# Kernel optimization log

Measured on AMD Instinct MI355X. Metric: run time of the kernel, lower is better.

Reference implementation:

```python
import jax, jax.numpy as jnp
import numpy as np

N = 50000      # nodes
E = 320000     # edges (before self-loops)
DIN = 128      # embedding_dim
D = 256        # intermediate_dim
H = 4          # heads_transformer
L = 2          # transformer_layers
NEG = 0.2      # LeakyReLU slope in GATConv


def setup_inputs() -> dict:
    key = jax.random.key(0)
    ks = jax.random.split(key, 16)
    def rn(k, shape, scale=0.05):
        return jax.random.normal(k, shape, jnp.float32) * scale
    return dict(
        x=jax.random.normal(ks[0], (N, DIN), jnp.float32),
        edge_index=jax.random.randint(ks[1], (2, E), 0, N),
        gat1_W=rn(ks[2], (D, DIN)), gat1_b=jnp.zeros((D,), jnp.float32),
        gat1_asrc=rn(ks[3], (D,)), gat1_adst=rn(ks[4], (D,)),
        gat2_W=rn(ks[5], (D, D)), gat2_b=jnp.zeros((D,), jnp.float32),
        gat2_asrc=rn(ks[6], (D,)), gat2_adst=rn(ks[7], (D,)),
        cls_token=rn(ks[8], (1, D)),
        pos_emb=rn(ks[9], (3, D)),
        Wqkv=rn(ks[10], (L, 3 * D, D)), bqkv=jnp.zeros((L, 3 * D), jnp.float32),
        Wo=rn(ks[11], (L, D, D)), bo=jnp.zeros((L, D), jnp.float32),
        ln1_g=jnp.ones((L, D), jnp.float32), ln1_b=jnp.zeros((L, D), jnp.float32),
        ln2_g=jnp.ones((L, D), jnp.float32), ln2_b=jnp.zeros((L, D), jnp.float32),
        Wff1=rn(ks[12], (L, 4 * D, D)), bff1=jnp.zeros((L, 4 * D), jnp.float32),
        Wff2=rn(ks[13], (L, D, 4 * D)), bff2=jnp.zeros((L, D), jnp.float32),
        norm_g=jnp.ones((D,), jnp.float32), norm_b=jnp.zeros((D,), jnp.float32),
    )


def layer_norm(x, g, b, eps=1e-5):
    m = jnp.mean(x, -1, keepdims=True)
    v = jnp.var(x, -1, keepdims=True)
    return (x - m) * jax.lax.rsqrt(v + eps) * g + b


def gat_conv(x, src, dst, W, b, a_src, a_dst):
    # PyG GATConv, heads=1, concat=False: h = xW^T; per-edge score
    # e = LeakyReLU(<h_src, a_src> + <h_dst, a_dst>); softmax grouped by dst.
    h = x @ W.T                                            # [N, D]
    e = jax.nn.leaky_relu((h @ a_src)[src] + (h @ a_dst)[dst], NEG)  # [E']
    m = jax.ops.segment_max(e, dst, num_segments=N)
    ex = jnp.exp(e - m[dst])
    denom = jax.ops.segment_sum(ex, dst, num_segments=N)
    alpha = ex / denom[dst]
    out = jax.ops.segment_sum(alpha[:, None] * h[src], dst, num_segments=N)
    return out + b


def mha(x, Wqkv, bqkv, Wo, bo):
    B, S, _ = x.shape
    dh = D // H
    qkv = x @ Wqkv.T + bqkv                                # [B, S, 3D]
    q, k, v = jnp.split(qkv, 3, axis=-1)
    q = q.reshape(B, S, H, dh); k = k.reshape(B, S, H, dh); v = v.reshape(B, S, H, dh)
    logits = jnp.einsum('bqhd,bkhd->bhqk', q, k) / jnp.sqrt(jnp.float32(dh))
    a = jax.nn.softmax(logits, -1)
    o = jnp.einsum('bhqk,bkhd->bqhd', a, v).reshape(B, S, D)
    return o @ Wo.T + bo


def reference(x, edge_index, gat1_W, gat1_b, gat1_asrc, gat1_adst,
              gat2_W, gat2_b, gat2_asrc, gat2_adst, cls_token, pos_emb,
              Wqkv, bqkv, Wo, bo, ln1_g, ln1_b, ln2_g, ln2_b,
              Wff1, bff1, Wff2, bff2, norm_g, norm_b):
    loops = jnp.arange(N)                                   # GATConv add_self_loops=True
    src = jnp.concatenate([edge_index[0], loops])
    dst = jnp.concatenate([edge_index[1], loops])

    x1 = jax.nn.relu(gat_conv(x, src, dst, gat1_W, gat1_b, gat1_asrc, gat1_adst))
    x2 = jax.nn.relu(gat_conv(x1, src, dst, gat2_W, gat2_b, gat2_asrc, gat2_adst))

    seq = jnp.concatenate([jnp.broadcast_to(cls_token, (N, 1, D)),
                           x1[:, None, :], x2[:, None, :]], axis=1)  # [N, 3, D]
    seq = seq + pos_emb                                     # broadcast [3, D]

    # post-norm TransformerEncoder (ReLU FFN, eval mode -> no dropout)
    for l in range(L):
        seq = layer_norm(seq + mha(seq, Wqkv[l], bqkv[l], Wo[l], bo[l]), ln1_g[l], ln1_b[l])
        ff = jax.nn.relu(seq @ Wff1[l].T + bff1[l]) @ Wff2[l].T + bff2[l]
        seq = layer_norm(seq + ff, ln2_g[l], ln2_b[l])

    seq = layer_norm(seq, norm_g, norm_b)
    return seq[:, 0, :]
```

## Files before the change

kernel.cpp:

```cpp
#include <hip/hip_runtime.h>
#include <hip/hip_bf16.h>

#define NN  50000
#define EE  320000
#define E2  (EE + NN)
#define DIN 128
#define DD  256

typedef __attribute__((ext_vector_type(8))) short          bf16x8;
typedef __attribute__((ext_vector_type(8))) unsigned short u16x8;
typedef __attribute__((ext_vector_type(4))) float          f32x4;


static __device__ __forceinline__ float bf2f(unsigned short u) {
  return __builtin_bit_cast(float, (unsigned)u << 16);
}

static __device__ __forceinline__ unsigned short f2bf(float f) {
  unsigned u = __builtin_bit_cast(unsigned, f);
  return (unsigned short)((u + 0x7fffu + ((u >> 16) & 1u)) >> 16);
}

static __device__ __forceinline__ void load_lds16(const void* g, void* l) {
  __builtin_amdgcn_global_load_lds(
      (const __attribute__((address_space(1))) void*)g,
      (__attribute__((address_space(3))) void*)l, 16, 0, 0);
}

static __device__ __forceinline__ float wredsum(float v) {
  for (int o = 32; o; o >>= 1) v += __shfl_xor(v, o);
  return v;
}


__global__ void k_cast(const float* __restrict__ in, unsigned short* __restrict__ out, int n) {
  int i = blockIdx.x * blockDim.x + threadIdx.x;
  if (i >= n) return;
  out[i] = f2bf(in[i]);
}


__global__ void k_deg(const int* __restrict__ ei, int* __restrict__ deg) {
  int i = blockIdx.x * blockDim.x + threadIdx.x;
  if (i >= E2) return;
  int dst = (i < EE) ? ei[EE + i] : (i - EE);
  atomicAdd(&deg[dst], 1);
}

__global__ __launch_bounds__(1024) void k_scan_tile(const int* __restrict__ in,
                                                    int* __restrict__ out,
                                                    int* __restrict__ tsum, int n) {
  __shared__ int sm[1024];
  int tid = threadIdx.x;
  int g = blockIdx.x * 1024 + tid;
  sm[tid] = (g < n) ? in[g] : 0;
  __syncthreads();
  for (int off = 1; off < 1024; off <<= 1) {
    int t = (tid >= off) ? sm[tid - off] : 0;
    __syncthreads();
    sm[tid] += t;
    __syncthreads();
  }
  if (g < n) out[g] = sm[tid];
  if (tid == 1023) tsum[blockIdx.x] = sm[1023];
}

__global__ void k_scan_sums(int* __restrict__ tsum, int nb) {
  int tid = threadIdx.x;
  int v = (tid < nb) ? tsum[tid] : 0;
  for (int off = 1; off < 64; off <<= 1) {
    int t = __shfl_up(v, off);
    if (tid >= off) v += t;
  }
  if (tid < nb) tsum[tid] = v;
}

__global__ void k_scan_add(int* __restrict__ out, const int* __restrict__ tsum, int n) {
  int g = blockIdx.x * blockDim.x + threadIdx.x;
  if (g >= n || g < 1024) return;
  out[g] += tsum[(g >> 10) - 1];
}

__global__ void k_scatter(const int* __restrict__ ei, const int* __restrict__ deg,
                          const int* __restrict__ inc, int* __restrict__ cur,
                          int* __restrict__ ssrc) {
  int i = blockIdx.x * blockDim.x + threadIdx.x;
  if (i >= E2) return;
  int src, dst;
  if (i < EE) { src = ei[i]; dst = ei[EE + i]; } else { src = dst = i - EE; }
  int pos = atomicAdd(&cur[dst], 1);
  ssrc[inc[dst] - deg[dst] + pos] = src;
}


__global__ __launch_bounds__(256) void k_dots(const unsigned short* __restrict__ hb,
                                              const float* __restrict__ asrc,
                                              const float* __restrict__ adst,
                                              float* __restrict__ hs, float* __restrict__ hd) {
  int node = blockIdx.x * 4 + (threadIdx.x >> 6);
  if (node >= NN) return;
  int lane = threadIdx.x & 63;
  ushort4 hv = *reinterpret_cast<const ushort4*>(hb + (size_t)node * DD + lane * 4);
  float v0 = bf2f(hv.x), v1 = bf2f(hv.y), v2 = bf2f(hv.z), v3 = bf2f(hv.w);
  const float* as = asrc + lane * 4;
  const float* ad = adst + lane * 4;
  float s1 = v0 * as[0] + v1 * as[1] + v2 * as[2] + v3 * as[3];
  float s2 = v0 * ad[0] + v1 * ad[1] + v2 * ad[2] + v3 * ad[3];
  for (int off = 32; off; off >>= 1) {
    s1 += __shfl_xor(s1, off);
    s2 += __shfl_xor(s2, off);
  }
  if (lane == 0) { hs[node] = s1; hd[node] = s2; }
}

__global__ __launch_bounds__(256) void k_gat(const unsigned short* __restrict__ hb,
                                             const int* __restrict__ ssrc,
                                             const int* __restrict__ deg,
                                             const int* __restrict__ inc,
                                             const float* __restrict__ hs,
                                             const float* __restrict__ hd,
                                             const float* __restrict__ bias,
                                             unsigned short* __restrict__ out) {
  __shared__ float sE[4][256];
  __shared__ int   sI[4][256];
  int w = threadIdx.x >> 6;
  int d = blockIdx.x * 4 + w;
  if (d >= NN) return;
  int lane = threadIdx.x & 63;
  int end = inc[d], cnt = deg[d], base = end - cnt;
  if (cnt > 256) cnt = 256;
  float hdd = hd[d];

  float m = -1e30f;
  for (int i0 = 0; i0 < cnt; i0 += 64) {
    int i = i0 + lane;
    float sc = -1e30f;
    if (i < cnt) {
      int s = ssrc[base + i];
      float v = hs[s] + hdd;
      sc = (v < 0.f) ? 0.2f * v : v;
      sI[w][i] = s;
      sE[w][i] = sc;
    }
    float mm = sc;
    for (int o = 32; o; o >>= 1) mm = fmaxf(mm, __shfl_xor(mm, o));
    m = fmaxf(m, mm);
  }
  float sum = 0.f;
  for (int i0 = 0; i0 < cnt; i0 += 64) {
    int i = i0 + lane;
    float e = 0.f;
    if (i < cnt) {
      e = __expf(sE[w][i] - m);
      sE[w][i] = e;
    }
    for (int o = 32; o; o >>= 1) e += __shfl_xor(e, o);
    sum += e;
  }
  float inv = 1.f / sum;

  float a0 = 0.f, a1 = 0.f, a2 = 0.f, a3 = 0.f;
  for (int i = 0; i < cnt; ++i) {
    float a = sE[w][i];
    int s = sI[w][i];
    ushort4 hv = *reinterpret_cast<const ushort4*>(hb + (size_t)s * DD + lane * 4);
    a0 += a * bf2f(hv.x);
    a1 += a * bf2f(hv.y);
    a2 += a * bf2f(hv.z);
    a3 += a * bf2f(hv.w);
  }
  const float* bp = bias + lane * 4;
  float r0 = a0 * inv + bp[0], r1 = a1 * inv + bp[1];
  float r2 = a2 * inv + bp[2], r3 = a3 * inv + bp[3];
  ushort4 o;
  o.x = f2bf(r0 > 0.f ? r0 : 0.f);
  o.y = f2bf(r1 > 0.f ? r1 : 0.f);
  o.z = f2bf(r2 > 0.f ? r2 : 0.f);
  o.w = f2bf(r3 > 0.f ? r3 : 0.f);
  *reinterpret_cast<ushort4*>(out + (size_t)d * DD + lane * 4) = o;
}



__global__ __launch_bounds__(512, 4) void k_gemmT(
    const unsigned short* __restrict__ A,
    const unsigned short* __restrict__ W,
    const float* __restrict__ bias,
    unsigned short* __restrict__ C,
    int M, int N, int K) {
  __shared__ unsigned short As[8 * 80 * 32];

  const int tid  = threadIdx.x;
  const int lane = tid & 63;
  const int w    = tid >> 6;
  const int ml   = lane & 15;
  const int quad = lane >> 4;
  const int m0   = blockIdx.x * 80;
  const int swz  = (quad ^ ((ml >> 1) & 3)) << 3;
  const int KG   = K >> 5;

  if (tid < 320) {
    int rg = m0 + (tid >> 2); if (rg >= M) rg = M - 1;
    int cs = (tid & 3) ^ ((tid >> 3) & 3);
    const unsigned short* gsrc = A + (size_t)rg * K + (cs << 3);
    unsigned short* ldst = As + (size_t)(w * 64) * 8;
    for (int g = 0; g < KG; ++g)
      load_lds16(gsrc + (g << 5), ldst + (size_t)g * 2560);
  }
  __syncthreads();

  const int nkb = N >> 8;
  for (int kb = 0; kb < nkb; ++kb) {
    f32x4 acc1[2][5] = {};
    const unsigned short* Wp = W + (size_t)(kb * 256 + w * 32 + ml) * K + quad * 8;
#pragma unroll 2
    for (int ks = 0; ks < KG; ++ks) {
      bf16x8 af[2], bg[5];
#pragma unroll
      for (int i = 0; i < 2; ++i)
        af[i] = *reinterpret_cast<const bf16x8*>(Wp + (size_t)i * 16 * K + ks * 32);
#pragma unroll
      for (int j = 0; j < 5; ++j)
        bg[j] = *reinterpret_cast<const bf16x8*>(&As[ks * 2560 + (j * 16 + ml) * 32 + swz]);
#pragma unroll
      for (int i = 0; i < 2; ++i)
#pragma unroll
        for (int j = 0; j < 5; ++j)
          acc1[i][j] = __builtin_amdgcn_mfma_f32_16x16x32_bf16(af[i], bg[j], acc1[i][j], 0, 0, 0);
    }

#pragma unroll
    for (int i = 0; i < 2; ++i) {
      int colb = kb * 256 + w * 32 + i * 16 + quad * 4;
      float4 bv = make_float4(0.f, 0.f, 0.f, 0.f);
      if (bias) bv = *reinterpret_cast<const float4*>(bias + colb);
#pragma unroll
      for (int j = 0; j < 5; ++j) {
        int rg = m0 + j * 16 + ml;
        if (rg < M) {
          ushort4 hv;
          hv.x = f2bf(acc1[i][j][0] + bv.x);
          hv.y = f2bf(acc1[i][j][1] + bv.y);
          hv.z = f2bf(acc1[i][j][2] + bv.z);
          hv.w = f2bf(acc1[i][j][3] + bv.w);
          *reinterpret_cast<ushort4*>(C + (size_t)rg * N + colb) = hv;
        }
      }
    }
  }
}


__global__ __launch_bounds__(256) void k_oproj(
    const unsigned short* __restrict__ qkvb,
    const unsigned short* __restrict__ Wo,
    const float* __restrict__ bo,
    const float* __restrict__ gam, const float* __restrict__ bet,
    unsigned short* __restrict__ seqc,
    int M) {
  __shared__ unsigned short As[8 * 48 * 32];
  __shared__ float sSum[4 * 48];
  __shared__ float sSq[4 * 48];

  const int tid  = threadIdx.x;
  const int lane = tid & 63;
  const int w    = tid >> 6;
  const int ml   = lane & 15;
  const int quad = lane >> 4;
  const int m0   = blockIdx.x * 48;
  const int swz  = (quad ^ ((ml >> 1) & 3)) * 8;

  const int d = lane;
  for (int i = 0; i < 4; ++i) {
    int r0 = (w * 4 + i) * 3;
    size_t rowg[3];
#pragma unroll
    for (int t = 0; t < 3; ++t) {
      int rg = m0 + r0 + t;
      rowg[t] = (size_t)(rg < M ? rg : M - 1);
    }
#pragma unroll
    for (int h = 0; h < 4; ++h) {
      float q[3], k[3], v[3];
#pragma unroll
      for (int t = 0; t < 3; ++t) {
        size_t base = rowg[t] * 768 + h * 64 + d;
        q[t] = bf2f(qkvb[base]);
        k[t] = bf2f(qkvb[base + 256]);
        v[t] = bf2f(qkvb[base + 512]);
      }
      float l[3][3];
#pragma unroll
      for (int a = 0; a < 3; ++a)
#pragma unroll
        for (int b = 0; b < 3; ++b)
          l[a][b] = wredsum(q[a] * k[b]) * 0.125f;
#pragma unroll
      for (int a = 0; a < 3; ++a) {
        float mx = fmaxf(l[a][0], fmaxf(l[a][1], l[a][2]));
        float e0 = __expf(l[a][0] - mx);
        float e1 = __expf(l[a][1] - mx);
        float e2 = __expf(l[a][2] - mx);
        float inv = 1.f / (e0 + e1 + e2);
        float o = (e0 * v[0] + e1 * v[1] + e2 * v[2]) * inv;
        int row = r0 + a;
        int col = h * 64 + d;
        int g = col >> 5, c = (col >> 3) & 3;
        As[((g * 48 + row) * 32) + ((c ^ ((row >> 1) & 3)) << 3) + (col & 7)] = f2bf(o);
      }
    }
  }
  __syncthreads();

  f32x4 acc[3][4] = {};
  const unsigned short* Wop = Wo + (size_t)(w * 64 + ml) * 256 + quad * 8;
#pragma unroll 2
  for (int t = 0; t < 8; ++t) {
    bf16x8 af[3], bg[4];
#pragma unroll
    for (int i = 0; i < 3; ++i)
      af[i] = *reinterpret_cast<const bf16x8*>(&As[(t * 48 + i * 16 + ml) * 32 + swz]);
#pragma unroll
    for (int j = 0; j < 4; ++j)
      bg[j] = *reinterpret_cast<const bf16x8*>(Wop + (size_t)j * 16 * 256 + t * 32);
#pragma unroll
    for (int i = 0; i < 3; ++i)
#pragma unroll
      for (int j = 0; j < 4; ++j)
        acc[i][j] = __builtin_amdgcn_mfma_f32_16x16x32_bf16(af[i], bg[j], acc[i][j], 0, 0, 0);
  }

  float bov[4], gv[4], btv[4];
#pragma unroll
  for (int j = 0; j < 4; ++j) {
    int col = w * 64 + j * 16 + ml;
    bov[j] = bo[col]; gv[j] = gam[col]; btv[j] = bet[col];
  }

#pragma unroll
  for (int i = 0; i < 3; ++i)
#pragma unroll
    for (int r = 0; r < 4; ++r) {
      int row = i * 16 + quad * 4 + r;
      int rg = m0 + row;
      size_t rr2 = (size_t)(rg < M ? rg : M - 1);
      float s = 0.f, s2 = 0.f;
#pragma unroll
      for (int j = 0; j < 4; ++j) {
        int col = w * 64 + j * 16 + ml;
        float t = acc[i][j][r] + bov[j] + bf2f(seqc[rr2 * 256 + col]);
        acc[i][j][r] = t;
        s += t; s2 += t * t;
      }
#pragma unroll
      for (int o = 1; o < 16; o <<= 1) { s += __shfl_xor(s, o); s2 += __shfl_xor(s2, o); }
      if (ml == 0) { sSum[w * 48 + row] = s; sSq[w * 48 + row] = s2; }
    }
  __syncthreads();

#pragma unroll
  for (int i = 0; i < 3; ++i)
#pragma unroll
    for (int r = 0; r < 4; ++r) {
      int row = i * 16 + quad * 4 + r;
      int rg = m0 + row;
      if (rg >= M) continue;
      float s  = sSum[row] + sSum[48 + row] + sSum[96 + row] + sSum[144 + row];
      float s2 = sSq[row]  + sSq[48 + row]  + sSq[96 + row]  + sSq[144 + row];
      float mean = s * (1.f / 256.f);
      float var  = s2 * (1.f / 256.f) - mean * mean;
      float inv  = rsqrtf(var + 1e-5f);
#pragma unroll
      for (int j = 0; j < 4; ++j) {
        int col = w * 64 + j * 16 + ml;
        seqc[(size_t)rg * 256 + col] = f2bf((acc[i][j][r] - mean) * inv * gv[j] + btv[j]);
      }
    }
}


__global__ __launch_bounds__(512, 4) void k_ff(
    unsigned short* __restrict__ A,
    const unsigned short* __restrict__ W1,
    const float* __restrict__ b1,
    const unsigned short* __restrict__ W2,
    const float* __restrict__ b2,
    const float* __restrict__ gam, const float* __restrict__ bet,
    int M) {
  __shared__ unsigned short As[8 * 80 * 32];
  __shared__ unsigned short Hs[8 * 80 * 32];

  const int tid  = threadIdx.x;
  const int lane = tid & 63;
  const int w    = tid >> 6;
  const int ml   = lane & 15;
  const int quad = lane >> 4;
  const int m0   = blockIdx.x * 80;
  const int swz  = (quad ^ ((ml >> 1) & 3)) << 3;

  if (tid < 320) {
    int rg = m0 + (tid >> 2); if (rg >= M) rg = M - 1;
    int cs = (tid & 3) ^ ((tid >> 3) & 3);
    const unsigned short* gsrc = A + (size_t)rg * 256 + (cs << 3);
    unsigned short* ldst = As + (size_t)(w * 64) * 8;
#pragma unroll
    for (int g = 0; g < 8; ++g)
      load_lds16(gsrc + (g << 5), ldst + (size_t)g * 2560);
  }
  __syncthreads();

  f32x4 acc2[5][2] = {};

  for (int kb = 0; kb < 4; ++kb) {
    f32x4 acc1[2][5] = {};
    const unsigned short* W1p = W1 + (size_t)(kb * 256 + w * 32 + ml) * 256 + quad * 8;
#pragma unroll 2
    for (int ks = 0; ks < 8; ++ks) {
      bf16x8 af[2], bg[5];
#pragma unroll
      for (int i = 0; i < 2; ++i)
        af[i] = *reinterpret_cast<const bf16x8*>(W1p + (size_t)i * 16 * 256 + ks * 32);
#pragma unroll
      for (int j = 0; j < 5; ++j)
        bg[j] = *reinterpret_cast<const bf16x8*>(&As[ks * 2560 + (j * 16 + ml) * 32 + swz]);
#pragma unroll
      for (int i = 0; i < 2; ++i)
#pragma unroll
        for (int j = 0; j < 5; ++j)
          acc1[i][j] = __builtin_amdgcn_mfma_f32_16x16x32_bf16(af[i], bg[j], acc1[i][j], 0, 0, 0);
    }

    __syncthreads();

#pragma unroll
    for (int i = 0; i < 2; ++i) {
      float4 bv = *reinterpret_cast<const float4*>(b1 + kb * 256 + w * 32 + i * 16 + quad * 4);
      int c  = i * 2 + (quad >> 1);
      int lo = (quad & 1) * 4;
#pragma unroll
      for (int j = 0; j < 5; ++j) {
        int seqrow = j * 16 + ml;
        int chsw = c ^ ((ml >> 1) & 3);
        int addr = w * 2560 + seqrow * 32 + (chsw << 3) + lo;
        float t0 = acc1[i][j][0] + bv.x; t0 = t0 > 0.f ? t0 : 0.f;
        float t1 = acc1[i][j][1] + bv.y; t1 = t1 > 0.f ? t1 : 0.f;
        float t2 = acc1[i][j][2] + bv.z; t2 = t2 > 0.f ? t2 : 0.f;
        float t3 = acc1[i][j][3] + bv.w; t3 = t3 > 0.f ? t3 : 0.f;
        ushort4 hv;
        hv.x = f2bf(t0); hv.y = f2bf(t1); hv.z = f2bf(t2); hv.w = f2bf(t3);
        *reinterpret_cast<ushort4*>(&Hs[addr]) = hv;
      }
    }
    __syncthreads();

    const unsigned short* W2p = W2 + (size_t)(w * 32 + ml) * 1024 + kb * 256 + quad * 8;
#pragma unroll 2
    for (int ks = 0; ks < 8; ++ks) {
      bf16x8 af[5], bg[2];
#pragma unroll
      for (int i = 0; i < 5; ++i)
        af[i] = *reinterpret_cast<const bf16x8*>(&Hs[ks * 2560 + (i * 16 + ml) * 32 + swz]);
#pragma unroll
      for (int j = 0; j < 2; ++j)
        bg[j] = *reinterpret_cast<const bf16x8*>(W2p + (size_t)j * 16 * 1024 + ks * 32);
#pragma unroll
      for (int i = 0; i < 5; ++i)
#pragma unroll
        for (int j = 0; j < 2; ++j)
          acc2[i][j] = __builtin_amdgcn_mfma_f32_16x16x32_bf16(af[i], bg[j], acc2[i][j], 0, 0, 0);
    }
  }

  __syncthreads();
  float* sS = reinterpret_cast<float*>(Hs);
  float* sQ = sS + 640;

  float b2v[2], gv[2], btv[2];
#pragma unroll
  for (int j = 0; j < 2; ++j) {
    int col = w * 32 + j * 16 + ml;
    b2v[j] = b2[col]; gv[j] = gam[col]; btv[j] = bet[col];
  }

#pragma unroll
  for (int i = 0; i < 5; ++i)
#pragma unroll
    for (int r = 0; r < 4; ++r) {
      int row = i * 16 + quad * 4 + r;
      float s = 0.f, s2 = 0.f;
#pragma unroll
      for (int j = 0; j < 2; ++j) {
        int c_r = j * 2 + (ml >> 3);
        float t = acc2[i][j][r] + b2v[j] +
                  bf2f(As[w * 2560 + row * 32 + ((c_r ^ ((row >> 1) & 3)) << 3) + (ml & 7)]);
        acc2[i][j][r] = t;
        s += t; s2 += t * t;
      }
#pragma unroll
      for (int o = 1; o < 16; o <<= 1) { s += __shfl_xor(s, o); s2 += __shfl_xor(s2, o); }
      if (ml == 0) { sS[w * 80 + row] = s; sQ[w * 80 + row] = s2; }
    }
  __syncthreads();

#pragma unroll
  for (int i = 0; i < 5; ++i)
#pragma unroll
    for (int r = 0; r < 4; ++r) {
      int row = i * 16 + quad * 4 + r;
      int rg = m0 + row;
      if (rg >= M) continue;
      float s = 0.f, s2 = 0.f;
#pragma unroll
      for (int ww = 0; ww < 8; ++ww) { s += sS[ww * 80 + row]; s2 += sQ[ww * 80 + row]; }
      float mean = s * (1.f / 256.f);
      float var  = s2 * (1.f / 256.f) - mean * mean;
      float inv  = rsqrtf(var + 1e-5f);
#pragma unroll
      for (int j = 0; j < 2; ++j) {
        int col = w * 32 + j * 16 + ml;
        A[(size_t)rg * 256 + col] = f2bf((acc2[i][j][r] - mean) * inv * gv[j] + btv[j]);
      }
    }
}


__global__ void k_seqbuild(const unsigned short* __restrict__ x1,
                           const unsigned short* __restrict__ x2,
                           const float* __restrict__ cls, const float* __restrict__ pos,
                           unsigned short* __restrict__ seqc, int n0, int cn) {
  int idx = blockIdx.x * blockDim.x + threadIdx.x;
  int total = cn * 3 * DD;
  if (idx >= total) return;
  int c = idx & (DD - 1);
  int r = idx >> 8;
  int t = r % 3, ln = r / 3;
  int n = n0 + ln;
  float v;
  if (t == 0)      v = cls[c];
  else if (t == 1) v = bf2f(x1[(size_t)n * DD + c]);
  else             v = bf2f(x2[(size_t)n * DD + c]);
  seqc[idx] = f2bf(v + pos[t * DD + c]);
}

__global__ __launch_bounds__(256) void k_final(const unsigned short* __restrict__ seqc,
                                               int n0, int cn,
                                               const float* __restrict__ g,
                                               const float* __restrict__ b,
                                               float* __restrict__ out) {
  int ln = blockIdx.x * 4 + (threadIdx.x >> 6);
  if (ln >= cn) return;
  int lane = threadIdx.x & 63;
  const unsigned short* p = seqc + (size_t)ln * 3 * DD;
  float v[4];
  float s = 0.f, s2 = 0.f;
#pragma unroll
  for (int i = 0; i < 4; ++i) {
    v[i] = bf2f(p[i * 64 + lane]);
    s += v[i]; s2 += v[i] * v[i];
  }
  for (int off = 32; off; off >>= 1) { s += __shfl_xor(s, off); s2 += __shfl_xor(s2, off); }
  float mean = s * (1.f / 256.f);
  float var  = s2 * (1.f / 256.f) - mean * mean;
  float inv  = rsqrtf(var + 1e-5f);
#pragma unroll
  for (int i = 0; i < 4; ++i) {
    int c = i * 64 + lane;
    out[(size_t)(n0 + ln) * DD + c] = (v[i] - mean) * inv * g[c] + b[c];
  }
}


extern "C" void kernel_launch(void* const* d_in, const int* in_sizes, int n_in,
                              void* d_out, int out_size, void* d_ws, size_t ws_size,
                              hipStream_t stream) {
  const float* x       = (const float*)d_in[0];
  const int*   ei      = (const int*)d_in[1];
  const float* gat1_W  = (const float*)d_in[2];
  const float* gat1_b  = (const float*)d_in[3];
  const float* gat1_as = (const float*)d_in[4];
  const float* gat1_ad = (const float*)d_in[5];
  const float* gat2_W  = (const float*)d_in[6];
  const float* gat2_b  = (const float*)d_in[7];
  const float* gat2_as = (const float*)d_in[8];
  const float* gat2_ad = (const float*)d_in[9];
  const float* cls     = (const float*)d_in[10];
  const float* pos     = (const float*)d_in[11];
  const float* Wqkv    = (const float*)d_in[12];
  const float* bqkv    = (const float*)d_in[13];
  const float* Wo      = (const float*)d_in[14];
  const float* bo      = (const float*)d_in[15];
  const float* ln1_g   = (const float*)d_in[16];
  const float* ln1_b   = (const float*)d_in[17];
  const float* ln2_g   = (const float*)d_in[18];
  const float* ln2_b   = (const float*)d_in[19];
  const float* Wff1    = (const float*)d_in[20];
  const float* bff1    = (const float*)d_in[21];
  const float* Wff2    = (const float*)d_in[22];
  const float* bff2    = (const float*)d_in[23];
  const float* norm_g  = (const float*)d_in[24];
  const float* norm_b  = (const float*)d_in[25];
  float* out = (float*)d_out;

  char* ws = (char*)d_ws;
  size_t off = 0;
  auto alloc = [&](size_t bytes) -> void* {
    off = (off + 255) & ~(size_t)255;
    void* p = ws + off;
    off += bytes;
    return p;
  };

  unsigned short* wb_g1  = (unsigned short*)alloc(sizeof(unsigned short) * 256 * 128);
  unsigned short* wb_g2  = (unsigned short*)alloc(sizeof(unsigned short) * 256 * 256);
  unsigned short* wb_qkv = (unsigned short*)alloc(sizeof(unsigned short) * 2 * 768 * 256);
  unsigned short* wb_o   = (unsigned short*)alloc(sizeof(unsigned short) * 2 * 256 * 256);
  unsigned short* wb_f1  = (unsigned short*)alloc(sizeof(unsigned short) * 2 * 1024 * 256);
  unsigned short* wb_f2  = (unsigned short*)alloc(sizeof(unsigned short) * 2 * 256 * 1024);
  unsigned short* xb  = (unsigned short*)alloc(sizeof(unsigned short) * (size_t)NN * DIN);
  unsigned short* hb  = (unsigned short*)alloc(sizeof(unsigned short) * (size_t)NN * DD);
  unsigned short* x1b = (unsigned short*)alloc(sizeof(unsigned short) * (size_t)NN * DD);
  unsigned short* x2b = (unsigned short*)alloc(sizeof(unsigned short) * (size_t)NN * DD);
  float* hs  = (float*)alloc(sizeof(float) * NN);
  float* hd  = (float*)alloc(sizeof(float) * NN);
  int* deg   = (int*)alloc(sizeof(int) * NN);
  int* inc   = (int*)alloc(sizeof(int) * NN);
  int* cur   = (int*)alloc(sizeof(int) * NN);
  int* tsum  = (int*)alloc(sizeof(int) * 64);
  int* ssrc  = (int*)alloc(sizeof(int) * E2);

  size_t fixed = (off + 255) & ~(size_t)255;
  size_t rem = (ws_size > fixed + 4096) ? (ws_size - fixed - 4096) : 0;
  const size_t per_node = (size_t)3 * (256 + 768) * 2;
  size_t cn_max = rem / per_node;
  if (cn_max < 1) cn_max = 1;
  if (cn_max > 12500) cn_max = 12500;
  int nc = (int)((NN + cn_max - 1) / cn_max);
  int cn = (NN + nc - 1) / nc;
  unsigned short* seqc = (unsigned short*)alloc(sizeof(unsigned short) * (size_t)3 * cn * 256);
  unsigned short* qkvb = (unsigned short*)alloc(sizeof(unsigned short) * (size_t)3 * cn * 768);

  auto cast = [&](const float* src, unsigned short* dst, int n) {
    k_cast<<<(n + 255) / 256, 256, 0, stream>>>(src, dst, n);
  };
  cast(gat1_W, wb_g1, 256 * 128);
  cast(gat2_W, wb_g2, 256 * 256);
  cast(Wqkv, wb_qkv, 2 * 768 * 256);
  cast(Wo, wb_o, 2 * 256 * 256);
  cast(Wff1, wb_f1, 2 * 1024 * 256);
  cast(Wff2, wb_f2, 2 * 256 * 1024);
  cast(x, xb, NN * DIN);

  hipMemsetAsync(deg, 0, sizeof(int) * NN, stream);
  hipMemsetAsync(cur, 0, sizeof(int) * NN, stream);
  k_deg<<<(E2 + 255) / 256, 256, 0, stream>>>(ei, deg);
  int nb = (NN + 1023) / 1024;
  k_scan_tile<<<nb, 1024, 0, stream>>>(deg, inc, tsum, NN);
  k_scan_sums<<<1, 64, 0, stream>>>(tsum, nb);
  k_scan_add<<<(NN + 255) / 256, 256, 0, stream>>>(inc, tsum, NN);
  k_scatter<<<(E2 + 255) / 256, 256, 0, stream>>>(ei, deg, inc, cur, ssrc);

  k_gemmT<<<(NN + 79) / 80, 512, 0, stream>>>(xb, wb_g1, nullptr, hb, NN, 256, 128);
  k_dots<<<(NN + 3) / 4, 256, 0, stream>>>(hb, gat1_as, gat1_ad, hs, hd);
  k_gat<<<(NN + 3) / 4, 256, 0, stream>>>(hb, ssrc, deg, inc, hs, hd, gat1_b, x1b);

  k_gemmT<<<(NN + 79) / 80, 512, 0, stream>>>(x1b, wb_g2, nullptr, hb, NN, 256, 256);
  k_dots<<<(NN + 3) / 4, 256, 0, stream>>>(hb, gat2_as, gat2_ad, hs, hd);
  k_gat<<<(NN + 3) / 4, 256, 0, stream>>>(hb, ssrc, deg, inc, hs, hd, gat2_b, x2b);

  for (int n0 = 0; n0 < NN; n0 += cn) {
    int c = NN - n0 < cn ? NN - n0 : cn;
    int Mch = 3 * c;
    int mblk48 = (Mch + 47) / 48;
    int mblk80 = (Mch + 79) / 80;
    k_seqbuild<<<(c * 3 * DD + 255) / 256, 256, 0, stream>>>(x1b, x2b, cls, pos, seqc, n0, c);
    for (int l = 0; l < 2; ++l) {
      k_gemmT<<<mblk80, 512, 0, stream>>>(
          seqc, wb_qkv + (size_t)l * 768 * 256, bqkv + l * 768, qkvb, Mch, 768, 256);
      k_oproj<<<mblk48, 256, 0, stream>>>(
          qkvb, wb_o + (size_t)l * 256 * 256, bo + l * 256,
          ln1_g + l * 256, ln1_b + l * 256, seqc, Mch);
      k_ff<<<mblk80, 512, 0, stream>>>(
          seqc, wb_f1 + (size_t)l * 1024 * 256, bff1 + l * 1024,
          wb_f2 + (size_t)l * 256 * 1024, bff2 + l * 256,
          ln2_g + l * 256, ln2_b + l * 256, Mch);
    }
    k_final<<<(c + 3) / 4, 256, 0, stream>>>(seqc, n0, c, norm_g, norm_b, out);
  }
}
```

Baseline: 1.914 ms.

## Vectorize attention loads, spread LDS tile loads across waves, raise MFMA priority

The attention kernel now has each lane load four contiguous bf16 values per row with ushort4 loads and covers all heads at once. The dot-product reduction shrinks from a full 64-lane reduction per head to a 16-lane xor shuffle tree, and results go to LDS as packed ushort4 stores. The A-tile global-to-LDS loads in the GEMM and FFN kernels are redistributed so every wave handles one K-chunk instead of 320 threads looping over all chunks. s_setprio(1) is placed around the MFMA loops to favour waves that are issuing matrix math. These touch several kernels, and the exact LDS address mapping must stay consistent with the swizzle used by the readers.

```diff
diff --git a/kernel.cpp b/kernel.cpp
--- a/kernel.cpp
+++ b/kernel.cpp
@@ -25,11 +25,6 @@
   __builtin_amdgcn_global_load_lds(
       (const __attribute__((address_space(1))) void*)g,
       (__attribute__((address_space(3))) void*)l, 16, 0, 0);
-}
-
-static __device__ __forceinline__ float wredsum(float v) {
-  for (int o = 32; o; o >>= 1) v += __shfl_xor(v, o);
-  return v;
 }
 
 
@@ -199,13 +194,16 @@
   const int swz  = (quad ^ ((ml >> 1) & 3)) << 3;
   const int KG   = K >> 5;
 
-  if (tid < 320) {
-    int rg = m0 + (tid >> 2); if (rg >= M) rg = M - 1;
-    int cs = (tid & 3) ^ ((tid >> 3) & 3);
-    const unsigned short* gsrc = A + (size_t)rg * K + (cs << 3);
-    unsigned short* ldst = As + (size_t)(w * 64) * 8;
-    for (int g = 0; g < KG; ++g)
-      load_lds16(gsrc + (g << 5), ldst + (size_t)g * 2560);
+  if (w < KG) {
+#pragma unroll
+    for (int r = 0; r < 5; ++r) {
+      int e = r * 64 + lane;
+      int row = e >> 2, ch = e & 3;
+      int rg = m0 + row; if (rg >= M) rg = M - 1;
+      int cs = ch ^ ((row >> 1) & 3);
+      load_lds16(A + (size_t)rg * K + w * 32 + (cs << 3),
+                 As + (size_t)(w * 320 + r * 64) * 8);
+    }
   }
   __syncthreads();
 
@@ -213,6 +211,7 @@
   for (int kb = 0; kb < nkb; ++kb) {
     f32x4 acc1[2][5] = {};
     const unsigned short* Wp = W + (size_t)(kb * 256 + w * 32 + ml) * K + quad * 8;
+    __builtin_amdgcn_s_setprio(1);
 #pragma unroll 2
     for (int ks = 0; ks < KG; ++ks) {
       bf16x8 af[2], bg[5];
@@ -228,6 +227,7 @@
         for (int j = 0; j < 5; ++j)
           acc1[i][j] = __builtin_amdgcn_mfma_f32_16x16x32_bf16(af[i], bg[j], acc1[i][j], 0, 0, 0);
     }
+    __builtin_amdgcn_s_setprio(0);
 
 #pragma unroll
     for (int i = 0; i < 2; ++i) {
@@ -270,7 +270,7 @@
   const int m0   = blockIdx.x * 48;
   const int swz  = (quad ^ ((ml >> 1) & 3)) * 8;
 
-  const int d = lane;
+  const int c0 = lane * 4;
   for (int i = 0; i < 4; ++i) {
     int r0 = (w * 4 + i) * 3;
     size_t rowg[3];
@@ -279,41 +279,54 @@
       int rg = m0 + r0 + t;
       rowg[t] = (size_t)(rg < M ? rg : M - 1);
     }
-#pragma unroll
-    for (int h = 0; h < 4; ++h) {
-      float q[3], k[3], v[3];
-#pragma unroll
-      for (int t = 0; t < 3; ++t) {
-        size_t base = rowg[t] * 768 + h * 64 + d;
-        q[t] = bf2f(qkvb[base]);
-        k[t] = bf2f(qkvb[base + 256]);
-        v[t] = bf2f(qkvb[base + 512]);
+    float q[3][4], k[3][4], v[3][4];
+#pragma unroll
+    for (int t = 0; t < 3; ++t) {
+      size_t base = rowg[t] * 768 + c0;
+      ushort4 uq = *reinterpret_cast<const ushort4*>(qkvb + base);
+      ushort4 uk = *reinterpret_cast<const ushort4*>(qkvb + base + 256);
+      ushort4 uv = *reinterpret_cast<const ushort4*>(qkvb + base + 512);
+      q[t][0] = bf2f(uq.x); q[t][1] = bf2f(uq.y); q[t][2] = bf2f(uq.z); q[t][3] = bf2f(uq.w);
+      k[t][0] = bf2f(uk.x); k[t][1] = bf2f(uk.y); k[t][2] = bf2f(uk.z); k[t][3] = bf2f(uk.w);
+      v[t][0] = bf2f(uv.x); v[t][1] = bf2f(uv.y); v[t][2] = bf2f(uv.z); v[t][3] = bf2f(uv.w);
+    }
+    float lg[3][3];
+#pragma unroll
+    for (int a = 0; a < 3; ++a)
+#pragma unroll
+      for (int b = 0; b < 3; ++b) {
+        float p = q[a][0] * k[b][0] + q[a][1] * k[b][1] +
+                  q[a][2] * k[b][2] + q[a][3] * k[b][3];
+        p += __shfl_xor(p, 1);
+        p += __shfl_xor(p, 2);
+        p += __shfl_xor(p, 4);
+        p += __shfl_xor(p, 8);
+        lg[a][b] = p * 0.125f;
       }
-      float l[3][3];
-#pragma unroll
-      for (int a = 0; a < 3; ++a)
-#pragma unroll
-        for (int b = 0; b < 3; ++b)
-          l[a][b] = wredsum(q[a] * k[b]) * 0.125f;
-#pragma unroll
-      for (int a = 0; a < 3; ++a) {
-        float mx = fmaxf(l[a][0], fmaxf(l[a][1], l[a][2]));
-        float e0 = __expf(l[a][0] - mx);
-        float e1 = __expf(l[a][1] - mx);
-        float e2 = __expf(l[a][2] - mx);
-        float inv = 1.f / (e0 + e1 + e2);
-        float o = (e0 * v[0] + e1 * v[1] + e2 * v[2]) * inv;
-        int row = r0 + a;
-        int col = h * 64 + d;
-        int g = col >> 5, c = (col >> 3) & 3;
-        As[((g * 48 + row) * 32) + ((c ^ ((row >> 1) & 3)) << 3) + (col & 7)] = f2bf(o);
-      }
+#pragma unroll
+    for (int a = 0; a < 3; ++a) {
+      float mx = fmaxf(lg[a][0], fmaxf(lg[a][1], lg[a][2]));
+      float e0 = __expf(lg[a][0] - mx);
+      float e1 = __expf(lg[a][1] - mx);
+      float e2 = __expf(lg[a][2] - mx);
+      float inv = 1.f / (e0 + e1 + e2);
+      int row = r0 + a;
+      int g = lane >> 3;
+      int cch = (lane >> 1) & 3;
+      int addr = (g * 48 + row) * 32 + ((cch ^ ((row >> 1) & 3)) << 3) + ((lane & 1) << 2);
+      ushort4 hv;
+      hv.x = f2bf((e0 * v[0][0] + e1 * v[1][0] + e2 * v[2][0]) * inv);
+      hv.y = f2bf((e0 * v[0][1] + e1 * v[1][1] + e2 * v[2][1]) * inv);
+      hv.z = f2bf((e0 * v[0][2] + e1 * v[1][2] + e2 * v[2][2]) * inv);
+      hv.w = f2bf((e0 * v[0][3] + e1 * v[1][3] + e2 * v[2][3]) * inv);
+      *reinterpret_cast<ushort4*>(&As[addr]) = hv;
     }
   }
   __syncthreads();
 
   f32x4 acc[3][4] = {};
   const unsigned short* Wop = Wo + (size_t)(w * 64 + ml) * 256 + quad * 8;
+  __builtin_amdgcn_s_setprio(1);
 #pragma unroll 2
   for (int t = 0; t < 8; ++t) {
     bf16x8 af[3], bg[4];
@@ -329,6 +342,7 @@
       for (int j = 0; j < 4; ++j)
         acc[i][j] = __builtin_amdgcn_mfma_f32_16x16x32_bf16(af[i], bg[j], acc[i][j], 0, 0, 0);
   }
+  __builtin_amdgcn_s_setprio(0);
 
   float bov[4], gv[4], btv[4];
 #pragma unroll
@@ -398,14 +412,16 @@
   const int m0   = blockIdx.x * 80;
   const int swz  = (quad ^ ((ml >> 1) & 3)) << 3;
 
-  if (tid < 320) {
-    int rg = m0 + (tid >> 2); if (rg >= M) rg = M - 1;
-    int cs = (tid & 3) ^ ((tid >> 3) & 3);
-    const unsigned short* gsrc = A + (size_t)rg * 256 + (cs << 3);
-    unsigned short* ldst = As + (size_t)(w * 64) * 8;
-#pragma unroll
-    for (int g = 0; g < 8; ++g)
-      load_lds16(gsrc + (g << 5), ldst + (size_t)g * 2560);
+  {
+#pragma unroll
+    for (int r = 0; r < 5; ++r) {
+      int e = r * 64 + lane;
+      int row = e >> 2, ch = e & 3;
+      int rg = m0 + row; if (rg >= M) rg = M - 1;
+      int cs = ch ^ ((row >> 1) & 3);
+      load_lds16(A + (size_t)rg * 256 + w * 32 + (cs << 3),
+                 As + (size_t)(w * 320 + r * 64) * 8);
+    }
   }
   __syncthreads();
 
@@ -414,6 +430,7 @@
   for (int kb = 0; kb < 4; ++kb) {
     f32x4 acc1[2][5] = {};
     const unsigned short* W1p = W1 + (size_t)(kb * 256 + w * 32 + ml) * 256 + quad * 8;
+    __builtin_amdgcn_s_setprio(1);
 #pragma unroll 2
     for (int ks = 0; ks < 8; ++ks) {
       bf16x8 af[2], bg[5];
@@ -429,6 +446,7 @@
         for (int j = 0; j < 5; ++j)
           acc1[i][j] = __builtin_amdgcn_mfma_f32_16x16x32_bf16(af[i], bg[j], acc1[i][j], 0, 0, 0);
     }
+    __builtin_amdgcn_s_setprio(0);
 
     __syncthreads();
 
@@ -454,6 +472,7 @@
     __syncthreads();
 
     const unsigned short* W2p = W2 + (size_t)(w * 32 + ml) * 1024 + kb * 256 + quad * 8;
+    __builtin_amdgcn_s_setprio(1);
 #pragma unroll 2
     for (int ks = 0; ks < 8; ++ks) {
       bf16x8 af[5], bg[2];
@@ -469,6 +488,7 @@
         for (int j = 0; j < 2; ++j)
           acc2[i][j] = __builtin_amdgcn_mfma_f32_16x16x32_bf16(af[i], bg[j], acc2[i][j], 0, 0, 0);
     }
+    __builtin_amdgcn_s_setprio(0);
   }
 
   __syncthreads();
```

Result: faster. 1.739 ms (-9.1%).
